# Optimization experiments

Hardware: AMD Instinct MI355X
Metric: run time of the kernel (lower is better)

## Reference

```python
import jax, jax.numpy as jnp
import numpy as np

B, N, D, H = 4, 2048, 1024, 16
HD = D // H
SCALE = D ** -0.5  # NOTE: original scales by dimension**-0.5 (not head_dim**-0.5)


def setup_inputs() -> dict:
    key = jax.random.key(0)
    k1, k2, k3 = jax.random.split(key, 3)
    x = jax.random.normal(k1, (B, N, D), dtype=jnp.float32)
    w_qkv = jax.random.normal(k2, (D, 3 * D), dtype=jnp.float32) * (D ** -0.5)
    w_proj = jax.random.normal(k3, (D, D), dtype=jnp.float32) * (D ** -0.5)
    b_proj = jnp.zeros((D,), dtype=jnp.float32)
    return {"x": x, "w_qkv": w_qkv, "w_proj": w_proj, "b_proj": b_proj}


def reference(x, w_qkv, w_proj, b_proj):
    # qkv projection: [B,N,3D] -> split into q,k,v each [B,H,N,HD]
    qkv = x @ w_qkv
    qkv = qkv.reshape(B, N, 3, H, HD).transpose(2, 0, 3, 1, 4)  # [3,B,H,N,HD]
    q, k, v = qkv[0], qkv[1], qkv[2]
    scores = jnp.einsum('bhid,bhjd->bhij', q, k) * SCALE
    attn = jax.nn.softmax(scores, axis=-1)
    out = jnp.einsum('bhij,bhjd->bhid', attn, v)  # [B,H,N,HD]
    out = out.transpose(0, 2, 1, 3).reshape(B, N, D)
    return out @ w_proj + b_proj
```

## Files before the change

kernel.cpp:

```cpp
#include <hip/hip_runtime.h>
#include <stdint.h>

#define Bdim 4
#define Nseq 2048
#define Dmod 1024
#define Hn   16
#define HD   64
#define SCALE 0.03125f
#define L2E   1.44269504089f

typedef __attribute__((ext_vector_type(8))) short short8;
typedef __attribute__((ext_vector_type(8))) unsigned short ushort8;
typedef __attribute__((ext_vector_type(4))) float f32x4;
typedef __attribute__((ext_vector_type(16))) float f32x16;

typedef __attribute__((address_space(3))) uint32_t lds_u32;
typedef __attribute__((address_space(1))) const uint32_t glob_u32;

static __device__ __forceinline__ void gload_lds16(const unsigned short* g, unsigned short* l) {
    __builtin_amdgcn_global_load_lds((glob_u32*)(const void*)g, (lds_u32*)(void*)l, 16, 0, 0);
}

static __device__ __forceinline__ unsigned short f2bf(float f) {
    union { float f; uint32_t u; } v; v.f = f;
    uint32_t r = (v.u + 0x7FFFu + ((v.u >> 16) & 1u)) >> 16;
    return (unsigned short)r;
}

__global__ __launch_bounds__(256) void cast_x_kernel(const float* __restrict__ in,
                                                     unsigned short* __restrict__ out, int n4) {
    int i = blockIdx.x * blockDim.x + threadIdx.x;
    int stride = gridDim.x * blockDim.x;
    for (; i < n4; i += stride) {
        float4 v = reinterpret_cast<const float4*>(in)[i];
        ushort4 o;
        o.x = f2bf(v.x); o.y = f2bf(v.y); o.z = f2bf(v.z); o.w = f2bf(v.w);
        reinterpret_cast<ushort4*>(out)[i] = o;
    }
}

__global__ void transpose_cast_kernel(const float* __restrict__ in,
                                      unsigned short* __restrict__ out, int R, int C) {
    __shared__ unsigned short t[32][33];
    int c0 = blockIdx.x * 32, r0 = blockIdx.y * 32;
    int tx = threadIdx.x, ty = threadIdx.y;
#pragma unroll
    for (int i = 0; i < 4; ++i)
        t[ty + i*8][tx] = f2bf(in[(size_t)(r0 + ty + i*8) * C + c0 + tx]);
    __syncthreads();
#pragma unroll
    for (int i = 0; i < 4; ++i)
        out[(size_t)(c0 + ty + i*8) * R + r0 + tx] = t[tx][ty + i*8];
}

template<bool OUT_BF16, bool BIAS, bool VSPLIT>
__global__ __launch_bounds__(256) void gemm_bt_kernel(const unsigned short* __restrict__ A,
                                                      const unsigned short* __restrict__ Bt,
                                                      void* __restrict__ Cv,
                                                      const float* __restrict__ bias,
                                                      unsigned short* __restrict__ vTp,
                                                      int M, int N, int K) {
    __shared__ unsigned short Al[128 * 64];
    __shared__ unsigned short Bl[128 * 64];
    int tid = threadIdx.x;
    int lane = tid & 63, wv = tid >> 6;
    int wr = (wv >> 1) * 64, wc = (wv & 1) * 64;
    int lr = lane & 15, lg = lane >> 4, lk = lg * 8;

    int gx = gridDim.x;
    int lin = blockIdx.y * gx + blockIdx.x;
    int cpx = (gx * gridDim.y) >> 3;
    int nl = (lin & 7) * cpx + (lin >> 3);
    int m0 = (nl / gx) * 128, n0 = (nl % gx) * 128;

    int srow = wv * 8 + (lane >> 3);
    int scol = (lane & 7) * 8;
    const unsigned short* ag = A  + (size_t)(m0 + srow) * K + scol;
    const unsigned short* bg = Bt + (size_t)(n0 + srow) * K + scol;
    unsigned short* la = Al + wv * 512;
    unsigned short* lb = Bl + wv * 512;

    f32x4 acc[4][4];
#pragma unroll
    for (int i = 0; i < 4; ++i)
#pragma unroll
        for (int j = 0; j < 4; ++j) acc[i][j] = (f32x4)0.f;

    for (int k0 = 0; k0 < K; k0 += 64) {
        __syncthreads();
#pragma unroll
        for (int i = 0; i < 4; ++i) {
            gload_lds16(ag + (size_t)i * 32 * K + k0, la + i * 2048);
            gload_lds16(bg + (size_t)i * 32 * K + k0, lb + i * 2048);
        }
        __syncthreads();
#pragma unroll
        for (int ks = 0; ks < 2; ++ks) {
            short8 a[4], b[4];
#pragma unroll
            for (int mi = 0; mi < 4; ++mi)
                a[mi] = *reinterpret_cast<const short8*>(Al + (wr + mi*16 + lr) * 64 + ks*32 + lk);
#pragma unroll
            for (int nj = 0; nj < 4; ++nj)
                b[nj] = *reinterpret_cast<const short8*>(Bl + (wc + nj*16 + lr) * 64 + ks*32 + lk);
#pragma unroll
            for (int mi = 0; mi < 4; ++mi)
#pragma unroll
                for (int nj = 0; nj < 4; ++nj)
                    acc[mi][nj] = __builtin_amdgcn_mfma_f32_16x16x32_bf16(a[mi], b[nj], acc[mi][nj], 0, 0, 0);
        }
    }
#pragma unroll
    for (int mi = 0; mi < 4; ++mi) {
#pragma unroll
        for (int nj = 0; nj < 4; ++nj) {
            int r = m0 + wr + mi*16 + lg*4;
            int c = n0 + wc + nj*16 + lr;
            if (VSPLIT && c >= 2048) {
                int cc = c - 2048;
                int bh = ((r >> 11) << 4) + (cc >> 6);
                int d = cc & 63;
                ushort4 o4;
                o4.x = f2bf(acc[mi][nj][0]);
                o4.y = f2bf(acc[mi][nj][1]);
                o4.z = f2bf(acc[mi][nj][2]);
                o4.w = f2bf(acc[mi][nj][3]);
                *reinterpret_cast<ushort4*>(vTp + ((size_t)(bh * 64 + d) * 2048) + (r & 2047)) = o4;
            } else {
                float bv = BIAS ? bias[c] : 0.f;
#pragma unroll
                for (int i = 0; i < 4; ++i) {
                    float v = acc[mi][nj][i] + bv;
                    if (OUT_BF16)
                        reinterpret_cast<unsigned short*>(Cv)[(size_t)(r + i) * N + c] = f2bf(v);
                    else
                        reinterpret_cast<float*>(Cv)[(size_t)(r + i) * N + c] = v;
                }
            }
        }
    }
}

__global__ __launch_bounds__(256, 2) void attn_kernel(const unsigned short* __restrict__ qkv,
                                                      const unsigned short* __restrict__ vT,
                                                      unsigned short* __restrict__ attn_o) {
    __shared__ unsigned short Kl[2 * 64 * 64];
    __shared__ unsigned short Vl[2 * 64 * 64];
    __shared__ unsigned short Pl[4 * 64 * 64];

    int w = blockIdx.x;
    int lid = (w & 7) * 64 + (w >> 3);
    int bh = lid >> 3, qb = lid & 7;
    int b = bh >> 4, h = bh & 15;

    int tid = threadIdx.x, lane = tid & 63, wv = tid >> 6;
    int lr = lane & 31, hi = lane >> 5;
    int q0 = qb * 256 + wv * 64;

    short8 qfA[4], qfB[4];
    {
        const unsigned short* qrowA = qkv + (size_t)(b * Nseq + q0 + lr) * 3072 + h * 64 + hi * 8;
        const unsigned short* qrowB = qrowA + (size_t)32 * 3072;
#pragma unroll
        for (int ks = 0; ks < 4; ++ks) {
            qfA[ks] = *reinterpret_cast<const short8*>(qrowA + ks * 16);
            qfB[ks] = *reinterpret_cast<const short8*>(qrowB + ks * 16);
        }
    }

    float mrunA = -1e30f, lrunA = 0.f, mrunB = -1e30f, lrunB = 0.f;
    f32x16 oA0 = (f32x16)0.f, oA1 = (f32x16)0.f, oB0 = (f32x16)0.f, oB1 = (f32x16)0.f;

    int sr = tid >> 2;
    const unsigned short* kg = qkv + (size_t)(b * Nseq + sr) * 3072 + 1024 + h * 64 + (tid & 3) * 16;
    const unsigned short* vg = vT + ((size_t)(bh * 64 + sr)) * Nseq + (tid & 3) * 16;
    int sb = (sr >> 5) * 4096 + (tid & 3) * 1024 + (sr & 31) * 16;
    char* Pw = (char*)Pl + wv * 8192 + lr * 16 + 8 * hi;
    char* Pr = (char*)Pl + wv * 8192 + lane * 16;

    {
        ushort8 a0 = *reinterpret_cast<const ushort8*>(kg);
        ushort8 a1 = *reinterpret_cast<const ushort8*>(kg + 8);
        ushort8 a2 = *reinterpret_cast<const ushort8*>(vg);
        ushort8 a3 = *reinterpret_cast<const ushort8*>(vg + 8);
        *reinterpret_cast<ushort8*>((char*)Kl + sb) = a0;
        *reinterpret_cast<ushort8*>((char*)Kl + sb + 512) = a1;
        *reinterpret_cast<ushort8*>((char*)Vl + sb) = a2;
        *reinterpret_cast<ushort8*>((char*)Vl + sb + 512) = a3;
    }
    ushort8 k0r = *reinterpret_cast<const ushort8*>(kg + (size_t)64 * 3072);
    ushort8 k1r = *reinterpret_cast<const ushort8*>(kg + (size_t)64 * 3072 + 8);
    ushort8 v0r = *reinterpret_cast<const ushort8*>(vg + 64);
    ushort8 v1r = *reinterpret_cast<const ushort8*>(vg + 72);

    int cur = 0;
    for (int jt = 0; jt < Nseq; jt += 64, cur ^= 1) {
        __syncthreads();
        int rb = cur * 8192, wb = rb ^ 8192;

        f32x16 sA0 = (f32x16)0.f, sA1 = (f32x16)0.f, sB0 = (f32x16)0.f, sB1 = (f32x16)0.f;
        __builtin_amdgcn_s_setprio(1);
#pragma unroll
        for (int ks = 0; ks < 4; ++ks) {
            short8 kf0 = *reinterpret_cast<const short8*>((char*)Kl + rb + ks*1024 + lane*16);
            short8 kf1 = *reinterpret_cast<const short8*>((char*)Kl + rb + 4096 + ks*1024 + lane*16);
            sA0 = __builtin_amdgcn_mfma_f32_32x32x16_bf16(kf0, qfA[ks], sA0, 0, 0, 0);
            sA1 = __builtin_amdgcn_mfma_f32_32x32x16_bf16(kf1, qfA[ks], sA1, 0, 0, 0);
            sB0 = __builtin_amdgcn_mfma_f32_32x32x16_bf16(kf0, qfB[ks], sB0, 0, 0, 0);
            sB1 = __builtin_amdgcn_mfma_f32_32x32x16_bf16(kf1, qfB[ks], sB1, 0, 0, 0);
        }
        __builtin_amdgcn_s_setprio(0);

        if (jt + 64 < Nseq) {
            *reinterpret_cast<ushort8*>((char*)Kl + wb + sb) = k0r;
            *reinterpret_cast<ushort8*>((char*)Kl + wb + sb + 512) = k1r;
            *reinterpret_cast<ushort8*>((char*)Vl + wb + sb) = v0r;
            *reinterpret_cast<ushort8*>((char*)Vl + wb + sb + 512) = v1r;
            int jn = jt + 128;
            if (jn < Nseq) {
                k0r = *reinterpret_cast<const ushort8*>(kg + (size_t)jn * 3072);
                k1r = *reinterpret_cast<const ushort8*>(kg + (size_t)jn * 3072 + 8);
                v0r = *reinterpret_cast<const ushort8*>(vg + jn);
                v1r = *reinterpret_cast<const ushort8*>(vg + jn + 8);
            }
        }

        float tA[16], tB[16];
#pragma unroll
        for (int i = 0; i < 16; ++i) { tA[i] = fmaxf(sA0[i], sA1[i]); tB[i] = fmaxf(sB0[i], sB1[i]); }
#pragma unroll
        for (int st = 8; st > 0; st >>= 1)
#pragma unroll
            for (int i = 0; i < st; ++i) { tA[i] = fmaxf(tA[i], tA[i + st]); tB[i] = fmaxf(tB[i], tB[i + st]); }
        float mlocA = fmaxf(tA[0], __shfl_xor(tA[0], 32)) * SCALE;
        float mlocB = fmaxf(tB[0], __shfl_xor(tB[0], 32)) * SCALE;

        if (!__all((mlocA <= mrunA + 8.f) && (mlocB <= mrunB + 8.f))) {
            float mnA = fmaxf(mrunA, mlocA);
            float fA = __builtin_amdgcn_exp2f((mrunA - mnA) * L2E);
            float mnB = fmaxf(mrunB, mlocB);
            float fB = __builtin_amdgcn_exp2f((mrunB - mnB) * L2E);
            lrunA *= fA; lrunB *= fB; mrunA = mnA; mrunB = mnB;
#pragma unroll
            for (int i = 0; i < 16; ++i) {
                oA0[i] *= fA; oA1[i] *= fA; oB0[i] *= fB; oB1[i] *= fB;
            }
        }

        const float c1 = SCALE * L2E;
        float c0A = -mrunA * L2E, c0B = -mrunB * L2E;
        float pA0[16], pA1[16], pB0[16], pB1[16];
#pragma unroll
        for (int i = 0; i < 16; ++i) {
            pA0[i] = __builtin_amdgcn_exp2f(fmaf(sA0[i], c1, c0A));
            pA1[i] = __builtin_amdgcn_exp2f(fmaf(sA1[i], c1, c0A));
            pB0[i] = __builtin_amdgcn_exp2f(fmaf(sB0[i], c1, c0B));
            pB1[i] = __builtin_amdgcn_exp2f(fmaf(sB1[i], c1, c0B));
        }

        uint32_t WA[16], WB[16];
#pragma unroll
        for (int m = 0; m < 8; ++m) {
            asm("v_cvt_pk_bf16_f32 %0, %1, %2" : "=v"(WA[m])   : "v"(pA0[2*m]), "v"(pA0[2*m+1]));
            asm("v_cvt_pk_bf16_f32 %0, %1, %2" : "=v"(WA[8+m]) : "v"(pA1[2*m]), "v"(pA1[2*m+1]));
            asm("v_cvt_pk_bf16_f32 %0, %1, %2" : "=v"(WB[m])   : "v"(pB0[2*m]), "v"(pB0[2*m+1]));
            asm("v_cvt_pk_bf16_f32 %0, %1, %2" : "=v"(WB[8+m]) : "v"(pB1[2*m]), "v"(pB1[2*m+1]));
        }
#pragma unroll
        for (int tt = 0; tt < 8; ++tt) {
            uint64_t valA = (uint64_t)WA[2*tt] | ((uint64_t)WA[2*tt+1] << 32);
            uint64_t valB = (uint64_t)WB[2*tt] | ((uint64_t)WB[2*tt+1] << 32);
            char* pa = Pw + (tt >> 1) * 1024 + (tt & 1) * 512;
            *reinterpret_cast<uint64_t*>(pa) = valA;
            *reinterpret_cast<uint64_t*>(pa + 4096) = valB;
        }

        float aA[16], aB[16];
#pragma unroll
        for (int i = 0; i < 16; ++i) { aA[i] = pA0[i] + pA1[i]; aB[i] = pB0[i] + pB1[i]; }
#pragma unroll
        for (int st = 8; st > 0; st >>= 1)
#pragma unroll
            for (int i = 0; i < st; ++i) { aA[i] += aA[i + st]; aB[i] += aB[i + st]; }
        lrunA += aA[0] + __shfl_xor(aA[0], 32);
        lrunB += aB[0] + __shfl_xor(aB[0], 32);

        __builtin_amdgcn_s_setprio(1);
#pragma unroll
        for (int ks4 = 0; ks4 < 4; ++ks4) {
            short8 vf0 = *reinterpret_cast<const short8*>((char*)Vl + rb + ks4*1024 + lane*16);
            short8 vf1 = *reinterpret_cast<const short8*>((char*)Vl + rb + 4096 + ks4*1024 + lane*16);
            short8 pfA = *reinterpret_cast<const short8*>(Pr + ks4*1024);
            short8 pfB = *reinterpret_cast<const short8*>(Pr + 4096 + ks4*1024);
            oA0 = __builtin_amdgcn_mfma_f32_32x32x16_bf16(vf0, pfA, oA0, 0, 0, 0);
            oA1 = __builtin_amdgcn_mfma_f32_32x32x16_bf16(vf1, pfA, oA1, 0, 0, 0);
            oB0 = __builtin_amdgcn_mfma_f32_32x32x16_bf16(vf0, pfB, oB0, 0, 0, 0);
            oB1 = __builtin_amdgcn_mfma_f32_32x32x16_bf16(vf1, pfB, oB1, 0, 0, 0);
        }
        __builtin_amdgcn_s_setprio(0);
    }

    float invA = 1.f / lrunA, invB = 1.f / lrunB;
    unsigned short* orowA = attn_o + (size_t)(b * Nseq + q0 + lr) * Dmod + h * 64;
    unsigned short* orowB = attn_o + (size_t)(b * Nseq + q0 + 32 + lr) * Dmod + h * 64;
#pragma unroll
    for (int db = 0; db < 2; ++db)
#pragma unroll
        for (int g = 0; g < 4; ++g) {
            int d = db * 32 + 8 * g + 4 * hi;
            ushort4 o4;
            o4.x = f2bf((db ? oA1[4*g+0] : oA0[4*g+0]) * invA);
            o4.y = f2bf((db ? oA1[4*g+1] : oA0[4*g+1]) * invA);
            o4.z = f2bf((db ? oA1[4*g+2] : oA0[4*g+2]) * invA);
            o4.w = f2bf((db ? oA1[4*g+3] : oA0[4*g+3]) * invA);
            *reinterpret_cast<ushort4*>(orowA + d) = o4;
            o4.x = f2bf((db ? oB1[4*g+0] : oB0[4*g+0]) * invB);
            o4.y = f2bf((db ? oB1[4*g+1] : oB0[4*g+1]) * invB);
            o4.z = f2bf((db ? oB1[4*g+2] : oB0[4*g+2]) * invB);
            o4.w = f2bf((db ? oB1[4*g+3] : oB0[4*g+3]) * invB);
            *reinterpret_cast<ushort4*>(orowB + d) = o4;
        }
}

extern "C" void kernel_launch(void* const* d_in, const int* in_sizes, int n_in,
                              void* d_out, int out_size, void* d_ws, size_t ws_size,
                              hipStream_t stream) {
    const float* x      = (const float*)d_in[0];
    const float* w_qkv  = (const float*)d_in[1];
    const float* w_proj = (const float*)d_in[2];
    const float* b_proj = (const float*)d_in[3];
    float* out = (float*)d_out;
    char* ws = (char*)d_ws;

    unsigned short* qkv    = (unsigned short*)(ws);
    unsigned short* vT     = (unsigned short*)(ws + 50331648);
    unsigned short* xb     = (unsigned short*)(ws + 67108864);
    unsigned short* attn_o = xb;
    unsigned short* wqkvT  = (unsigned short*)(ws + 83886080);
    unsigned short* wprojT = (unsigned short*)(ws + 90177536);

    cast_x_kernel<<<2048, 256, 0, stream>>>(x, xb, (Bdim*Nseq*Dmod)/4);
    transpose_cast_kernel<<<dim3(3072/32, 1024/32), dim3(32, 8), 0, stream>>>(w_qkv, wqkvT, 1024, 3072);
    transpose_cast_kernel<<<dim3(1024/32, 1024/32), dim3(32, 8), 0, stream>>>(w_proj, wprojT, 1024, 1024);
    gemm_bt_kernel<true, false, true><<<dim3(3072/128, 8192/128), 256, 0, stream>>>(
        xb, wqkvT, qkv, nullptr, vT, Bdim*Nseq, 3*Dmod, Dmod);
    attn_kernel<<<512, 256, 0, stream>>>(qkv, vT, attn_o);
    gemm_bt_kernel<false, true, false><<<dim3(1024/128, 8192/128), 256, 0, stream>>>(
        attn_o, wprojT, out, b_proj, nullptr, Bdim*Nseq, Dmod, Dmod);
}
```

Measured before the change: 223.9 us.

## Shrink attention tile to 32 query rows per wave and keep P in registers

The attention kernel now gives each wave 32 query rows instead of 64 and each block 128 rows, and launches 1024 blocks with a four-blocks-per-CU launch bound. The P tile no longer goes through shared memory; it is rearranged with cross-half-wave shuffles into the MFMA B-operand layout. K/V tiles are loaded by direct global-to-LDS loads. Together these aim to cut LDS traffic and raise occupancy and latency hiding, at the cost of re-reading K/V twice as often per query and adding shuffles.

New measurement: 232.4 us. 1.04x slower.

```diff
diff --git a/kernel.cpp b/kernel.cpp
--- a/kernel.cpp
+++ b/kernel.cpp
@@ -141,184 +141,154 @@
     }
 }
 
-__global__ __launch_bounds__(256, 2) void attn_kernel(const unsigned short* __restrict__ qkv,
+__global__ __launch_bounds__(256, 4) void attn_kernel(const unsigned short* __restrict__ qkv,
                                                       const unsigned short* __restrict__ vT,
                                                       unsigned short* __restrict__ attn_o) {
     __shared__ unsigned short Kl[2 * 64 * 64];
     __shared__ unsigned short Vl[2 * 64 * 64];
-    __shared__ unsigned short Pl[4 * 64 * 64];
 
     int w = blockIdx.x;
-    int lid = (w & 7) * 64 + (w >> 3);
-    int bh = lid >> 3, qb = lid & 7;
+    int lid = (w & 7) * 128 + (w >> 3);
+    int bh = lid >> 4, qb = lid & 15;
     int b = bh >> 4, h = bh & 15;
 
     int tid = threadIdx.x, lane = tid & 63, wv = tid >> 6;
     int lr = lane & 31, hi = lane >> 5;
-    int q0 = qb * 256 + wv * 64;
-
-    short8 qfA[4], qfB[4];
+    int q0 = qb * 128 + wv * 32;
+
+    short8 qf[4];
     {
-        const unsigned short* qrowA = qkv + (size_t)(b * Nseq + q0 + lr) * 3072 + h * 64 + hi * 8;
-        const unsigned short* qrowB = qrowA + (size_t)32 * 3072;
-#pragma unroll
-        for (int ks = 0; ks < 4; ++ks) {
-            qfA[ks] = *reinterpret_cast<const short8*>(qrowA + ks * 16);
-            qfB[ks] = *reinterpret_cast<const short8*>(qrowB + ks * 16);
-        }
-    }
-
-    float mrunA = -1e30f, lrunA = 0.f, mrunB = -1e30f, lrunB = 0.f;
-    f32x16 oA0 = (f32x16)0.f, oA1 = (f32x16)0.f, oB0 = (f32x16)0.f, oB1 = (f32x16)0.f;
-
-    int sr = tid >> 2;
-    const unsigned short* kg = qkv + (size_t)(b * Nseq + sr) * 3072 + 1024 + h * 64 + (tid & 3) * 16;
-    const unsigned short* vg = vT + ((size_t)(bh * 64 + sr)) * Nseq + (tid & 3) * 16;
-    int sb = (sr >> 5) * 4096 + (tid & 3) * 1024 + (sr & 31) * 16;
-    char* Pw = (char*)Pl + wv * 8192 + lr * 16 + 8 * hi;
-    char* Pr = (char*)Pl + wv * 8192 + lane * 16;
+        const unsigned short* qrow = qkv + (size_t)(b * Nseq + q0 + lr) * 3072 + h * 64 + hi * 8;
+#pragma unroll
+        for (int ks = 0; ks < 4; ++ks)
+            qf[ks] = *reinterpret_cast<const short8*>(qrow + ks * 16);
+    }
+
+    float mrun = -1e30f, lrun = 0.f;
+    f32x16 o0 = (f32x16)0.f, o1 = (f32x16)0.f;
+
+    int c0 = wv * 128 + lane, c1 = c0 + 64;
+    int kv0 = ((c0 >> 8) << 5) + (c0 & 31), d00 = (((c0 >> 6) & 3) << 4) + (((c0 >> 5) & 1) << 3);
+    int kv1 = ((c1 >> 8) << 5) + (c1 & 31), d01 = (((c1 >> 6) & 3) << 4) + (((c1 >> 5) & 1) << 3);
+    const unsigned short* kp0 = qkv + (size_t)(b * Nseq + kv0) * 3072 + 1024 + h * 64 + d00;
+    const unsigned short* kp1 = qkv + (size_t)(b * Nseq + kv1) * 3072 + 1024 + h * 64 + d01;
+    const unsigned short* vp0 = vT + ((size_t)(bh * 64 + kv0)) * Nseq + d00;
+    const unsigned short* vp1 = vT + ((size_t)(bh * 64 + kv1)) * Nseq + d01;
 
     {
-        ushort8 a0 = *reinterpret_cast<const ushort8*>(kg);
-        ushort8 a1 = *reinterpret_cast<const ushort8*>(kg + 8);
-        ushort8 a2 = *reinterpret_cast<const ushort8*>(vg);
-        ushort8 a3 = *reinterpret_cast<const ushort8*>(vg + 8);
-        *reinterpret_cast<ushort8*>((char*)Kl + sb) = a0;
-        *reinterpret_cast<ushort8*>((char*)Kl + sb + 512) = a1;
-        *reinterpret_cast<ushort8*>((char*)Vl + sb) = a2;
-        *reinterpret_cast<ushort8*>((char*)Vl + sb + 512) = a3;
-    }
-    ushort8 k0r = *reinterpret_cast<const ushort8*>(kg + (size_t)64 * 3072);
-    ushort8 k1r = *reinterpret_cast<const ushort8*>(kg + (size_t)64 * 3072 + 8);
-    ushort8 v0r = *reinterpret_cast<const ushort8*>(vg + 64);
-    ushort8 v1r = *reinterpret_cast<const ushort8*>(vg + 72);
-
-    int cur = 0;
-    for (int jt = 0; jt < Nseq; jt += 64, cur ^= 1) {
-        __syncthreads();
-        int rb = cur * 8192, wb = rb ^ 8192;
-
-        f32x16 sA0 = (f32x16)0.f, sA1 = (f32x16)0.f, sB0 = (f32x16)0.f, sB1 = (f32x16)0.f;
+        unsigned short* kd = (unsigned short*)((char*)Kl + wv * 2048);
+        unsigned short* vd = (unsigned short*)((char*)Vl + wv * 2048);
+        gload_lds16(kp0, kd);  gload_lds16(kp1, (unsigned short*)((char*)kd + 1024));
+        gload_lds16(vp0, vd);  gload_lds16(vp1, (unsigned short*)((char*)vd + 1024));
+        kp0 += 64 * 3072; kp1 += 64 * 3072; vp0 += 64; vp1 += 64;
+    }
+    __syncthreads();
+
+    for (int t = 0; t < 32; ++t) {
+        int rb = (t & 1) * 8192;
+
+        if (t < 31) {
+            unsigned short* kd = (unsigned short*)((char*)Kl + (rb ^ 8192) + wv * 2048);
+            unsigned short* vd = (unsigned short*)((char*)Vl + (rb ^ 8192) + wv * 2048);
+            gload_lds16(kp0, kd);  gload_lds16(kp1, (unsigned short*)((char*)kd + 1024));
+            gload_lds16(vp0, vd);  gload_lds16(vp1, (unsigned short*)((char*)vd + 1024));
+            kp0 += 64 * 3072; kp1 += 64 * 3072; vp0 += 64; vp1 += 64;
+        }
+
+        f32x16 s0 = (f32x16)0.f, s1 = (f32x16)0.f;
         __builtin_amdgcn_s_setprio(1);
 #pragma unroll
         for (int ks = 0; ks < 4; ++ks) {
             short8 kf0 = *reinterpret_cast<const short8*>((char*)Kl + rb + ks*1024 + lane*16);
             short8 kf1 = *reinterpret_cast<const short8*>((char*)Kl + rb + 4096 + ks*1024 + lane*16);
-            sA0 = __builtin_amdgcn_mfma_f32_32x32x16_bf16(kf0, qfA[ks], sA0, 0, 0, 0);
-            sA1 = __builtin_amdgcn_mfma_f32_32x32x16_bf16(kf1, qfA[ks], sA1, 0, 0, 0);
-            sB0 = __builtin_amdgcn_mfma_f32_32x32x16_bf16(kf0, qfB[ks], sB0, 0, 0, 0);
-            sB1 = __builtin_amdgcn_mfma_f32_32x32x16_bf16(kf1, qfB[ks], sB1, 0, 0, 0);
+            s0 = __builtin_amdgcn_mfma_f32_32x32x16_bf16(kf0, qf[ks], s0, 0, 0, 0);
+            s1 = __builtin_amdgcn_mfma_f32_32x32x16_bf16(kf1, qf[ks], s1, 0, 0, 0);
         }
         __builtin_amdgcn_s_setprio(0);
 
-        if (jt + 64 < Nseq) {
-            *reinterpret_cast<ushort8*>((char*)Kl + wb + sb) = k0r;
-            *reinterpret_cast<ushort8*>((char*)Kl + wb + sb + 512) = k1r;
-            *reinterpret_cast<ushort8*>((char*)Vl + wb + sb) = v0r;
-            *reinterpret_cast<ushort8*>((char*)Vl + wb + sb + 512) = v1r;
-            int jn = jt + 128;
-            if (jn < Nseq) {
-                k0r = *reinterpret_cast<const ushort8*>(kg + (size_t)jn * 3072);
-                k1r = *reinterpret_cast<const ushort8*>(kg + (size_t)jn * 3072 + 8);
-                v0r = *reinterpret_cast<const ushort8*>(vg + jn);
-                v1r = *reinterpret_cast<const ushort8*>(vg + jn + 8);
-            }
-        }
-
-        float tA[16], tB[16];
-#pragma unroll
-        for (int i = 0; i < 16; ++i) { tA[i] = fmaxf(sA0[i], sA1[i]); tB[i] = fmaxf(sB0[i], sB1[i]); }
+        float tmx[16];
+#pragma unroll
+        for (int i = 0; i < 16; ++i) tmx[i] = fmaxf(s0[i], s1[i]);
 #pragma unroll
         for (int st = 8; st > 0; st >>= 1)
 #pragma unroll
-            for (int i = 0; i < st; ++i) { tA[i] = fmaxf(tA[i], tA[i + st]); tB[i] = fmaxf(tB[i], tB[i + st]); }
-        float mlocA = fmaxf(tA[0], __shfl_xor(tA[0], 32)) * SCALE;
-        float mlocB = fmaxf(tB[0], __shfl_xor(tB[0], 32)) * SCALE;
-
-        if (!__all((mlocA <= mrunA + 8.f) && (mlocB <= mrunB + 8.f))) {
-            float mnA = fmaxf(mrunA, mlocA);
-            float fA = __builtin_amdgcn_exp2f((mrunA - mnA) * L2E);
-            float mnB = fmaxf(mrunB, mlocB);
-            float fB = __builtin_amdgcn_exp2f((mrunB - mnB) * L2E);
-            lrunA *= fA; lrunB *= fB; mrunA = mnA; mrunB = mnB;
-#pragma unroll
-            for (int i = 0; i < 16; ++i) {
-                oA0[i] *= fA; oA1[i] *= fA; oB0[i] *= fB; oB1[i] *= fB;
-            }
-        }
-
-        const float c1 = SCALE * L2E;
-        float c0A = -mrunA * L2E, c0B = -mrunB * L2E;
-        float pA0[16], pA1[16], pB0[16], pB1[16];
+            for (int i = 0; i < st; ++i) tmx[i] = fmaxf(tmx[i], tmx[i + st]);
+        float mloc = fmaxf(tmx[0], __shfl_xor(tmx[0], 32)) * SCALE;
+
+        if (!__all(mloc <= mrun + 8.f)) {
+            float mn = fmaxf(mrun, mloc);
+            float fc = __builtin_amdgcn_exp2f((mrun - mn) * L2E);
+            lrun *= fc; mrun = mn;
+#pragma unroll
+            for (int i = 0; i < 16; ++i) { o0[i] *= fc; o1[i] *= fc; }
+        }
+
+        const float c1f = SCALE * L2E;
+        float c0f = -mrun * L2E;
 #pragma unroll
         for (int i = 0; i < 16; ++i) {
-            pA0[i] = __builtin_amdgcn_exp2f(fmaf(sA0[i], c1, c0A));
-            pA1[i] = __builtin_amdgcn_exp2f(fmaf(sA1[i], c1, c0A));
-            pB0[i] = __builtin_amdgcn_exp2f(fmaf(sB0[i], c1, c0B));
-            pB1[i] = __builtin_amdgcn_exp2f(fmaf(sB1[i], c1, c0B));
-        }
-
-        uint32_t WA[16], WB[16];
+            s0[i] = __builtin_amdgcn_exp2f(fmaf(s0[i], c1f, c0f));
+            s1[i] = __builtin_amdgcn_exp2f(fmaf(s1[i], c1f, c0f));
+        }
+
+        float a[16];
+#pragma unroll
+        for (int i = 0; i < 16; ++i) a[i] = s0[i] + s1[i];
+#pragma unroll
+        for (int st = 8; st > 0; st >>= 1)
+#pragma unroll
+            for (int i = 0; i < st; ++i) a[i] += a[i + st];
+        lrun += a[0] + __shfl_xor(a[0], 32);
+
+        uint32_t U[16];
 #pragma unroll
         for (int m = 0; m < 8; ++m) {
-            asm("v_cvt_pk_bf16_f32 %0, %1, %2" : "=v"(WA[m])   : "v"(pA0[2*m]), "v"(pA0[2*m+1]));
-            asm("v_cvt_pk_bf16_f32 %0, %1, %2" : "=v"(WA[8+m]) : "v"(pA1[2*m]), "v"(pA1[2*m+1]));
-            asm("v_cvt_pk_bf16_f32 %0, %1, %2" : "=v"(WB[m])   : "v"(pB0[2*m]), "v"(pB0[2*m+1]));
-            asm("v_cvt_pk_bf16_f32 %0, %1, %2" : "=v"(WB[8+m]) : "v"(pB1[2*m]), "v"(pB1[2*m+1]));
-        }
-#pragma unroll
-        for (int tt = 0; tt < 8; ++tt) {
-            uint64_t valA = (uint64_t)WA[2*tt] | ((uint64_t)WA[2*tt+1] << 32);
-            uint64_t valB = (uint64_t)WB[2*tt] | ((uint64_t)WB[2*tt+1] << 32);
-            char* pa = Pw + (tt >> 1) * 1024 + (tt & 1) * 512;
-            *reinterpret_cast<uint64_t*>(pa) = valA;
-            *reinterpret_cast<uint64_t*>(pa + 4096) = valB;
-        }
-
-        float aA[16], aB[16];
-#pragma unroll
-        for (int i = 0; i < 16; ++i) { aA[i] = pA0[i] + pA1[i]; aB[i] = pB0[i] + pB1[i]; }
-#pragma unroll
-        for (int st = 8; st > 0; st >>= 1)
-#pragma unroll
-            for (int i = 0; i < st; ++i) { aA[i] += aA[i + st]; aB[i] += aB[i + st]; }
-        lrunA += aA[0] + __shfl_xor(aA[0], 32);
-        lrunB += aB[0] + __shfl_xor(aB[0], 32);
+            asm("v_cvt_pk_bf16_f32 %0, %1, %2" : "=v"(U[m])   : "v"(s0[2*m]), "v"(s0[2*m+1]));
+            asm("v_cvt_pk_bf16_f32 %0, %1, %2" : "=v"(U[8+m]) : "v"(s1[2*m]), "v"(s1[2*m+1]));
+        }
+        uint32_t rv[8];
+#pragma unroll
+        for (int g = 0; g < 2; ++g) {
+            const int oo = g * 8, ro = g * 4;
+            rv[ro+0] = (uint32_t)__shfl_xor((int)(hi ? U[oo+0] : U[oo+2]), 32);
+            rv[ro+1] = (uint32_t)__shfl_xor((int)(hi ? U[oo+1] : U[oo+3]), 32);
+            rv[ro+2] = (uint32_t)__shfl_xor((int)(hi ? U[oo+4] : U[oo+6]), 32);
+            rv[ro+3] = (uint32_t)__shfl_xor((int)(hi ? U[oo+5] : U[oo+7]), 32);
+        }
 
         __builtin_amdgcn_s_setprio(1);
 #pragma unroll
         for (int ks4 = 0; ks4 < 4; ++ks4) {
+            const int hh = 8*(ks4>>1) + 4*(ks4&1);
+            const int rc = 4*(ks4>>1) + 2*(ks4&1);
+            union { uint32_t u[4]; short8 s; } f;
+            f.u[0] = hi ? rv[rc]    : U[hh];
+            f.u[1] = hi ? rv[rc+1]  : U[hh+1];
+            f.u[2] = hi ? U[hh+2]   : rv[rc];
+            f.u[3] = hi ? U[hh+3]   : rv[rc+1];
             short8 vf0 = *reinterpret_cast<const short8*>((char*)Vl + rb + ks4*1024 + lane*16);
             short8 vf1 = *reinterpret_cast<const short8*>((char*)Vl + rb + 4096 + ks4*1024 + lane*16);
-            short8 pfA = *reinterpret_cast<const short8*>(Pr + ks4*1024);
-            short8 pfB = *reinterpret_cast<const short8*>(Pr + 4096 + ks4*1024);
-            oA0 = __builtin_amdgcn_mfma_f32_32x32x16_bf16(vf0, pfA, oA0, 0, 0, 0);
-            oA1 = __builtin_amdgcn_mfma_f32_32x32x16_bf16(vf1, pfA, oA1, 0, 0, 0);
-            oB0 = __builtin_amdgcn_mfma_f32_32x32x16_bf16(vf0, pfB, oB0, 0, 0, 0);
-            oB1 = __builtin_amdgcn_mfma_f32_32x32x16_bf16(vf1, pfB, oB1, 0, 0, 0);
+            o0 = __builtin_amdgcn_mfma_f32_32x32x16_bf16(vf0, f.s, o0, 0, 0, 0);
+            o1 = __builtin_amdgcn_mfma_f32_32x32x16_bf16(vf1, f.s, o1, 0, 0, 0);
         }
         __builtin_amdgcn_s_setprio(0);
-    }
-
-    float invA = 1.f / lrunA, invB = 1.f / lrunB;
-    unsigned short* orowA = attn_o + (size_t)(b * Nseq + q0 + lr) * Dmod + h * 64;
-    unsigned short* orowB = attn_o + (size_t)(b * Nseq + q0 + 32 + lr) * Dmod + h * 64;
+
+        __syncthreads();
+    }
+
+    float inv = 1.f / lrun;
+    unsigned short* orow = attn_o + (size_t)(b * Nseq + q0 + lr) * Dmod + h * 64;
 #pragma unroll
     for (int db = 0; db < 2; ++db)
 #pragma unroll
         for (int g = 0; g < 4; ++g) {
             int d = db * 32 + 8 * g + 4 * hi;
             ushort4 o4;
-            o4.x = f2bf((db ? oA1[4*g+0] : oA0[4*g+0]) * invA);
-            o4.y = f2bf((db ? oA1[4*g+1] : oA0[4*g+1]) * invA);
-            o4.z = f2bf((db ? oA1[4*g+2] : oA0[4*g+2]) * invA);
-            o4.w = f2bf((db ? oA1[4*g+3] : oA0[4*g+3]) * invA);
-            *reinterpret_cast<ushort4*>(orowA + d) = o4;
-            o4.x = f2bf((db ? oB1[4*g+0] : oB0[4*g+0]) * invB);
-            o4.y = f2bf((db ? oB1[4*g+1] : oB0[4*g+1]) * invB);
-            o4.z = f2bf((db ? oB1[4*g+2] : oB0[4*g+2]) * invB);
-            o4.w = f2bf((db ? oB1[4*g+3] : oB0[4*g+3]) * invB);
-            *reinterpret_cast<ushort4*>(orowB + d) = o4;
+            o4.x = f2bf((db ? o1[4*g+0] : o0[4*g+0]) * inv);
+            o4.y = f2bf((db ? o1[4*g+1] : o0[4*g+1]) * inv);
+            o4.z = f2bf((db ? o1[4*g+2] : o0[4*g+2]) * inv);
+            o4.w = f2bf((db ? o1[4*g+3] : o0[4*g+3]) * inv);
+            *reinterpret_cast<ushort4*>(orow + d) = o4;
         }
 }
 
@@ -344,7 +314,7 @@
     transpose_cast_kernel<<<dim3(1024/32, 1024/32), dim3(32, 8), 0, stream>>>(w_proj, wprojT, 1024, 1024);
     gemm_bt_kernel<true, false, true><<<dim3(3072/128, 8192/128), 256, 0, stream>>>(
         xb, wqkvT, qkv, nullptr, vT, Bdim*Nseq, 3*Dmod, Dmod);
-    attn_kernel<<<512, 256, 0, stream>>>(qkv, vT, attn_o);
+    attn_kernel<<<1024, 256, 0, stream>>>(qkv, vT, attn_o);
     gemm_bt_kernel<false, true, false><<<dim3(1024/128, 8192/128), 256, 0, stream>>>(
         attn_o, wprojT, out, b_proj, nullptr, Bdim*Nseq, Dmod, Dmod);
 }
```
